# Kernel tuning notes

Hardware: AMD Instinct MI355X
Metric: run time of the kernel (lower is better)

Reference implementation:

```python
import jax, jax.numpy as jnp
import numpy as np

N_TOKENS = 2048
D_IN = 1024
D_HID = 4096
D_OUT = 1024
N_EXPERTS = 8
TOP_K = 2


def setup_inputs() -> dict:
    key = jax.random.key(0)
    ks = jax.random.split(key, 8)
    s_in = 1.0 / np.sqrt(D_IN)
    s_hid = 1.0 / np.sqrt(D_HID)
    return {
        "x": jax.random.normal(ks[0], (N_TOKENS, D_IN), dtype=jnp.float32),
        # Router Linear(D_IN, E)
        "Wr": jax.random.uniform(ks[1], (D_IN, N_EXPERTS), jnp.float32, -s_in, s_in),
        "br": jax.random.uniform(ks[2], (N_EXPERTS,), jnp.float32, -s_in, s_in),
        # Stacked expert MLP weights [E, ...]
        "W1": jax.random.uniform(ks[3], (N_EXPERTS, D_IN, D_HID), jnp.float32, -s_in, s_in),
        "b1": jax.random.uniform(ks[4], (N_EXPERTS, D_HID), jnp.float32, -s_in, s_in),
        "W2": jax.random.uniform(ks[5], (N_EXPERTS, D_HID, D_OUT), jnp.float32, -s_hid, s_hid),
        "b2": jax.random.uniform(ks[6], (N_EXPERTS, D_OUT), jnp.float32, -s_hid, s_hid),
    }


def reference(x, Wr, br, W1, b1, W2, b2):
    # Router: softmax over expert logits, then top-k
    routing = jax.nn.softmax(x @ Wr + br, axis=-1)            # [N, E]
    topk_w, topk_idx = jax.lax.top_k(routing, TOP_K)          # [N, k] each
    # Combine weights per expert: c[n, e] = sum_i topk_w[n, i] * (topk_idx[n, i] == e)
    onehot = jax.nn.one_hot(topk_idx, N_EXPERTS, dtype=x.dtype)  # [N, k, E]
    combine = jnp.einsum('nk,nke->ne', topk_w, onehot)           # [N, E]
    # Run all experts on all tokens (dense equivalent of the dispatch loop);
    # non-selected experts get combine weight 0, so math matches exactly.
    h = jax.nn.relu(jnp.einsum('nd,edh->neh', x, W1) + b1)       # [N, E, H]
    y = jnp.einsum('neh,ehd->ned', h, W2) + b2                   # [N, E, Dout]
    out = jnp.einsum('ne,ned->nd', combine, y)                   # [N, Dout]
    return out
```

## Files before the change

### kernel.cpp

```cpp
#include <hip/hip_runtime.h>
#include <hip/hip_bf16.h>

#define N_TOKENS 2048
#define D_IN 1024
#define D_HID 4096
#define D_OUT 1024
#define NE 8

typedef __attribute__((ext_vector_type(8))) short s16x8;
typedef __attribute__((ext_vector_type(4))) float f32x4;

__device__ inline unsigned short f2bf(float f) {
  union { float f; unsigned u; } v; v.f = f;
  unsigned u = v.u;
  unsigned r = u + 0x7fff + ((u >> 16) & 1);
  return (unsigned short)(r >> 16);
}

#define GLDS16(gp, lp)                                                          \
  __builtin_amdgcn_global_load_lds(                                             \
      (const __attribute__((address_space(1))) unsigned int*)(gp),              \
      (__attribute__((address_space(3))) unsigned int*)(lp), 16, 0, 0)

__global__ __launch_bounds__(256) void router_kernel(
    const float* __restrict__ x, const float* __restrict__ Wr,
    const float* __restrict__ br, int* __restrict__ cnt, int* __restrict__ tids,
    int4* __restrict__ meta, float2* __restrict__ tw) {
  int wid = threadIdx.x >> 6, lane = threadIdx.x & 63;
  int n = blockIdx.x * 4 + wid;
  const float* xr = x + (size_t)n * D_IN;
  float acc[NE];
#pragma unroll
  for (int e = 0; e < NE; e++) acc[e] = 0.f;
  for (int i = lane; i < D_IN; i += 64) {
    float xv = xr[i];
    const float4* wr = (const float4*)(Wr + (size_t)i * NE);
    float4 w0 = wr[0], w1 = wr[1];
    acc[0] += xv * w0.x; acc[1] += xv * w0.y;
    acc[2] += xv * w0.z; acc[3] += xv * w0.w;
    acc[4] += xv * w1.x; acc[5] += xv * w1.y;
    acc[6] += xv * w1.z; acc[7] += xv * w1.w;
  }
#pragma unroll
  for (int e = 0; e < NE; e++) {
#pragma unroll
    for (int s = 32; s; s >>= 1) acc[e] += __shfl_xor(acc[e], s, 64);
  }
  if (lane == 0) {
    float lg[NE], p[NE];
    float m = -1e30f;
#pragma unroll
    for (int e = 0; e < NE; e++) { lg[e] = acc[e] + br[e]; m = fmaxf(m, lg[e]); }
    float s = 0.f;
#pragma unroll
    for (int e = 0; e < NE; e++) { p[e] = expf(lg[e] - m); s += p[e]; }
    float inv = 1.f / s;
    int i0 = 0;
#pragma unroll
    for (int e = 1; e < NE; e++) if (lg[e] > lg[i0]) i0 = e;
    int i1 = (i0 == 0) ? 1 : 0;
#pragma unroll
    for (int e = 0; e < NE; e++) if (e != i0 && lg[e] > lg[i1]) i1 = e;
    int p0 = atomicAdd(&cnt[i0], 1);
    int p1 = atomicAdd(&cnt[i1], 1);
    tids[i0 * N_TOKENS + p0] = n;
    tids[i1 * N_TOKENS + p1] = n;
    meta[n] = make_int4(i0, p0, i1, p1);
    tw[n] = make_float2(p[i0] * inv, p[i1] * inv);
  }
}

__global__ __launch_bounds__(256) void convx_kernel(const float* __restrict__ x,
                                                    short* __restrict__ xb) {
  int i = (blockIdx.x * 256 + threadIdx.x) * 4;
  float4 v = *(const float4*)(x + i);
  short4 o;
  o.x = (short)f2bf(v.x); o.y = (short)f2bf(v.y);
  o.z = (short)f2bf(v.z); o.w = (short)f2bf(v.w);
  *(short4*)(xb + i) = o;
}

__global__ __launch_bounds__(256) void transconv_kernel(
    const float* __restrict__ src, short* __restrict__ dst, int R, int C) {
  __shared__ float tile[64][65];
  size_t eoff = (size_t)blockIdx.z * R * C;
  int r0 = blockIdx.y * 64, c0 = blockIdx.x * 64;
  const float* s = src + eoff + (size_t)r0 * C + c0;
  int t = threadIdx.x;
  int lc4 = (t & 15) * 4;
  int lr16 = t >> 4;
#pragma unroll
  for (int p = 0; p < 4; p++) {
    int r = p * 16 + lr16;
    float4 v = *(const float4*)(s + (size_t)r * C + lc4);
    tile[r][lc4 + 0] = v.x; tile[r][lc4 + 1] = v.y;
    tile[r][lc4 + 2] = v.z; tile[r][lc4 + 3] = v.w;
  }
  __syncthreads();
  short* d = dst + eoff + (size_t)c0 * R + r0;
  int rr4 = (t & 15) * 4;
  int cc = t >> 4;
#pragma unroll
  for (int p = 0; p < 4; p++) {
    int c = p * 16 + cc;
    short4 o;
    o.x = (short)f2bf(tile[rr4 + 0][c]);
    o.y = (short)f2bf(tile[rr4 + 1][c]);
    o.z = (short)f2bf(tile[rr4 + 2][c]);
    o.w = (short)f2bf(tile[rr4 + 3][c]);
    *(short4*)(d + (size_t)c * R + rr4) = o;
  }
}

__global__ __launch_bounds__(256) void gemm1_kernel(
    const short* __restrict__ xb,
    const short* __restrict__ W1b,
    const float* __restrict__ b1,
    const int* __restrict__ cnt, const int* __restrict__ tids,
    short* __restrict__ H) {
  const int NT_M = N_TOKENS / 128, NT_N = D_HID / 128;
  int bid0 = blockIdx.x;
  int bid = (bid0 & 7) * ((NE * NT_M * NT_N) >> 3) + (bid0 >> 3);
  int e = bid / (NT_M * NT_N);
  int r2 = bid % (NT_M * NT_N);
  int mt = r2 % NT_M, nt = r2 / NT_M;
  int ce = cnt[e];
  if (mt * 128 >= ce) return;
  int off = 0;
  for (int i = 0; i < e; i++) off += cnt[i];

  __shared__ alignas(16) short As[2][128][64];
  __shared__ alignas(16) short Bs[2][128][64];

  int lane = threadIdx.x & 63, wid = threadIdx.x >> 6;
  int wr = wid >> 1, wc = wid & 1;
  int lrow = lane >> 3;
  int ach = ((lane & 7) ^ lrow) * 8;

  const int* tlist = tids + e * N_TOKENS + mt * 128;
  const short* agp[4];
  const short* bgp[4];
#pragma unroll
  for (int c = 0; c < 4; c++) {
    int r = c * 32 + wid * 8 + lrow;
    int t = (mt * 128 + r < ce) ? tlist[r] : tlist[0];
    agp[c] = xb + (size_t)t * D_IN + ach;
    bgp[c] = W1b + (size_t)e * D_HID * D_IN + (size_t)(nt * 128 + r) * D_IN + ach;
  }

  f32x4 zero = {0.f, 0.f, 0.f, 0.f};
  f32x4 acc[4][4];
#pragma unroll
  for (int i = 0; i < 4; i++) {
#pragma unroll
    for (int j = 0; j < 4; j++) acc[i][j] = zero;
  }

#define STAGE1(ks, buf)                                                         \
  {                                                                             \
    int k0 = (ks) * 64;                                                         \
    _Pragma("unroll")                                                           \
    for (int c = 0; c < 4; c++) {                                               \
      GLDS16(agp[c] + k0, &As[buf][c * 32 + wid * 8][0]);                       \
      GLDS16(bgp[c] + k0, &Bs[buf][c * 32 + wid * 8][0]);                       \
    }                                                                           \
  }

  const int NK = D_IN / 64;
  STAGE1(0, 0);
  STAGE1(1, 1);
  int cur = 0;
  for (int ks = 0; ks < NK; ks++) {
    if (ks + 1 < NK) asm volatile("s_waitcnt vmcnt(8)" : : : "memory");
    else             asm volatile("s_waitcnt vmcnt(0)" : : : "memory");
    __builtin_amdgcn_s_barrier();
#pragma unroll
    for (int kk = 0; kk < 2; kk++) {
      s16x8 a[4], b[4];
      int ch = ((kk * 4 + (lane >> 4)) ^ (lane & 7)) * 8;
#pragma unroll
      for (int i = 0; i < 4; i++)
        a[i] = *(const s16x8*)&As[cur][wr * 64 + i * 16 + (lane & 15)][ch];
#pragma unroll
      for (int j = 0; j < 4; j++)
        b[j] = *(const s16x8*)&Bs[cur][wc * 64 + j * 16 + (lane & 15)][ch];
#pragma unroll
      for (int i = 0; i < 4; i++) {
#pragma unroll
        for (int j = 0; j < 4; j++)
          acc[i][j] = __builtin_amdgcn_mfma_f32_16x16x32_bf16(a[i], b[j], acc[i][j], 0, 0, 0);
      }
    }
    __builtin_amdgcn_s_barrier();
    if (ks + 2 < NK) STAGE1(ks + 2, cur);
    cur ^= 1;
  }

  int lr = (lane >> 4) * 4, lc = lane & 15;
#pragma unroll
  for (int j = 0; j < 4; j++) {
    int col = nt * 128 + wc * 64 + j * 16 + lc;
    float bias = b1[e * D_HID + col];
#pragma unroll
    for (int i = 0; i < 4; i++) {
#pragma unroll
      for (int r = 0; r < 4; r++) {
        int grow = mt * 128 + wr * 64 + i * 16 + lr + r;
        if (grow < ce) {
          float v = fmaxf(acc[i][j][r] + bias, 0.f);
          H[(size_t)(off + grow) * D_HID + col] = (short)f2bf(v);
        }
      }
    }
  }
}

__global__ __launch_bounds__(256) void gemm2_kernel(
    const short* __restrict__ H,
    const short* __restrict__ W2b,
    const int* __restrict__ cnt,
    float* __restrict__ Y) {
  const int NT_M = N_TOKENS / 128, NT_N = D_OUT / 128;
  int bid0 = blockIdx.x;
  int bid = (bid0 & 7) * ((NE * NT_M * NT_N) >> 3) + (bid0 >> 3);
  int e = bid / (NT_M * NT_N);
  int r2 = bid % (NT_M * NT_N);
  int mt = r2 % NT_M, nt = r2 / NT_M;
  int ce = cnt[e];
  if (mt * 128 >= ce) return;
  int off = 0;
  for (int i = 0; i < e; i++) off += cnt[i];

  __shared__ alignas(16) short As[2][128][64];
  __shared__ alignas(16) short Bs[2][128][64];

  int lane = threadIdx.x & 63, wid = threadIdx.x >> 6;
  int wr = wid >> 1, wc = wid & 1;
  int lrow = lane >> 3;
  int ach = ((lane & 7) ^ lrow) * 8;

  const short* agp[4];
  const short* bgp[4];
#pragma unroll
  for (int c = 0; c < 4; c++) {
    int r = c * 32 + wid * 8 + lrow;
    int grow = mt * 128 + r;
    if (grow > ce - 1) grow = ce - 1;
    agp[c] = H + (size_t)(off + grow) * D_HID + ach;
    bgp[c] = W2b + (size_t)e * D_OUT * D_HID + (size_t)(nt * 128 + r) * D_HID + ach;
  }

  f32x4 zero = {0.f, 0.f, 0.f, 0.f};
  f32x4 acc[4][4];
#pragma unroll
  for (int i = 0; i < 4; i++) {
#pragma unroll
    for (int j = 0; j < 4; j++) acc[i][j] = zero;
  }

#define STAGE2(ks, buf)                                                         \
  {                                                                             \
    int k0 = (ks) * 64;                                                         \
    _Pragma("unroll")                                                           \
    for (int c = 0; c < 4; c++) {                                               \
      GLDS16(agp[c] + k0, &As[buf][c * 32 + wid * 8][0]);                       \
      GLDS16(bgp[c] + k0, &Bs[buf][c * 32 + wid * 8][0]);                       \
    }                                                                           \
  }

  const int NK = D_HID / 64;
  STAGE2(0, 0);
  STAGE2(1, 1);
  int cur = 0;
  for (int ks = 0; ks < NK; ks++) {
    if (ks + 1 < NK) asm volatile("s_waitcnt vmcnt(8)" : : : "memory");
    else             asm volatile("s_waitcnt vmcnt(0)" : : : "memory");
    __builtin_amdgcn_s_barrier();
#pragma unroll
    for (int kk = 0; kk < 2; kk++) {
      s16x8 a[4], b[4];
      int ch = ((kk * 4 + (lane >> 4)) ^ (lane & 7)) * 8;
#pragma unroll
      for (int i = 0; i < 4; i++)
        a[i] = *(const s16x8*)&As[cur][wr * 64 + i * 16 + (lane & 15)][ch];
#pragma unroll
      for (int j = 0; j < 4; j++)
        b[j] = *(const s16x8*)&Bs[cur][wc * 64 + j * 16 + (lane & 15)][ch];
#pragma unroll
      for (int i = 0; i < 4; i++) {
#pragma unroll
        for (int j = 0; j < 4; j++)
          acc[i][j] = __builtin_amdgcn_mfma_f32_16x16x32_bf16(a[i], b[j], acc[i][j], 0, 0, 0);
      }
    }
    __builtin_amdgcn_s_barrier();
    if (ks + 2 < NK) STAGE2(ks + 2, cur);
    cur ^= 1;
  }

  int lr = (lane >> 4) * 4, lc = lane & 15;
#pragma unroll
  for (int j = 0; j < 4; j++) {
    int col = nt * 128 + wc * 64 + j * 16 + lc;
#pragma unroll
    for (int i = 0; i < 4; i++) {
#pragma unroll
      for (int r = 0; r < 4; r++) {
        int grow = mt * 128 + wr * 64 + i * 16 + lr + r;
        if (grow < ce) Y[(size_t)(off + grow) * D_OUT + col] = acc[i][j][r];
      }
    }
  }
}

__global__ __launch_bounds__(256) void combine_kernel(
    const float* __restrict__ Y, const float* __restrict__ b2,
    const int* __restrict__ cnt, const int4* __restrict__ meta,
    const float2* __restrict__ tw, float* __restrict__ out) {
  int n = blockIdx.x;
  int4 m = meta[n];
  float2 w = tw[n];
  int off0 = 0, off1 = 0;
#pragma unroll
  for (int i = 0; i < NE; i++) {
    int c = cnt[i];
    if (i < m.x) off0 += c;
    if (i < m.z) off1 += c;
  }
  const float4* y0 = (const float4*)(Y + (size_t)(off0 + m.y) * D_OUT);
  const float4* y1 = (const float4*)(Y + (size_t)(off1 + m.w) * D_OUT);
  const float4* g0 = (const float4*)(b2 + (size_t)m.x * D_OUT);
  const float4* g1 = (const float4*)(b2 + (size_t)m.z * D_OUT);
  float4* o = (float4*)(out + (size_t)n * D_OUT);
  int d = threadIdx.x;
  float4 a = y0[d], b = y1[d], ba = g0[d], bb = g1[d];
  float4 r;
  r.x = w.x * (a.x + ba.x) + w.y * (b.x + bb.x);
  r.y = w.x * (a.y + ba.y) + w.y * (b.y + bb.y);
  r.z = w.x * (a.z + ba.z) + w.y * (b.z + bb.z);
  r.w = w.x * (a.w + ba.w) + w.y * (b.w + bb.w);
  o[d] = r;
}

extern "C" void kernel_launch(void* const* d_in, const int* in_sizes, int n_in,
                              void* d_out, int out_size, void* d_ws, size_t ws_size,
                              hipStream_t stream) {
  const float* x  = (const float*)d_in[0];
  const float* Wr = (const float*)d_in[1];
  const float* br = (const float*)d_in[2];
  const float* W1 = (const float*)d_in[3];
  const float* b1 = (const float*)d_in[4];
  const float* W2 = (const float*)d_in[5];
  const float* b2 = (const float*)d_in[6];
  float* out = (float*)d_out;

  char* ws = (char*)d_ws;
  size_t o = 0;
  auto alloc = [&](size_t bytes) -> void* {
    o = (o + 255) & ~(size_t)255;
    void* p = ws + o;
    o += bytes;
    return p;
  };
  int*    cnt  = (int*)alloc(NE * 4);
  int*    tids = (int*)alloc((size_t)NE * N_TOKENS * 4);
  int4*   meta = (int4*)alloc((size_t)N_TOKENS * 16);
  float2* tw   = (float2*)alloc((size_t)N_TOKENS * 8);
  short*  xb   = (short*)alloc((size_t)N_TOKENS * D_IN * 2);
  short*  W1b  = (short*)alloc((size_t)NE * D_HID * D_IN * 2);
  short*  W2b  = (short*)alloc((size_t)NE * D_OUT * D_HID * 2);
  short*  H    = (short*)alloc((size_t)2 * N_TOKENS * D_HID * 2);
  float*  Y    = (float*)alloc((size_t)2 * N_TOKENS * D_OUT * 4);
  if (o > ws_size) return;

  hipMemsetAsync(cnt, 0, NE * 4, stream);
  router_kernel<<<N_TOKENS / 4, 256, 0, stream>>>(x, Wr, br, cnt, tids, meta, tw);
  convx_kernel<<<(N_TOKENS * D_IN / 4) / 256, 256, 0, stream>>>(x, xb);
  transconv_kernel<<<dim3(D_HID / 64, D_IN / 64, NE), 256, 0, stream>>>(W1, W1b, D_IN, D_HID);
  transconv_kernel<<<dim3(D_OUT / 64, D_HID / 64, NE), 256, 0, stream>>>(W2, W2b, D_HID, D_OUT);
  gemm1_kernel<<<NE * (N_TOKENS / 128) * (D_HID / 128), 256, 0, stream>>>(xb, W1b, b1, cnt, tids, H);
  gemm2_kernel<<<NE * (N_TOKENS / 128) * (D_OUT / 128), 256, 0, stream>>>(H, W2b, cnt, Y);
  combine_kernel<<<N_TOKENS, 256, 0, stream>>>(Y, b2, cnt, meta, tw, out);
}
```

Before: 579.2 us.

## Split-K gemm2 into two halves and shrink K-tile to 32

The gemm2 kernel now splits the 4096-long hidden reduction into two halves, launching twice as many blocks. Each half writes its own partial Y buffer, and the combine kernel sums the two partials. Both GEMMs also drop the LDS K-tile from 64 to 32, halving shared memory per block with a new XOR swizzle. The aim is more parallelism for the under-occupied gemm2 grid and higher occupancy. The cost is extra Y traffic, a doubled workspace, and twice as many barriers per unit of K.

```diff
diff --git a/kernel.cpp b/kernel.cpp
--- a/kernel.cpp
+++ b/kernel.cpp
@@ -129,68 +129,63 @@
   int off = 0;
   for (int i = 0; i < e; i++) off += cnt[i];
 
-  __shared__ alignas(16) short As[2][128][64];
-  __shared__ alignas(16) short Bs[2][128][64];
+  __shared__ alignas(16) short As[2][128][32];
+  __shared__ alignas(16) short Bs[2][128][32];
 
   int lane = threadIdx.x & 63, wid = threadIdx.x >> 6;
   int wr = wid >> 1, wc = wid & 1;
-  int lrow = lane >> 3;
-  int ach = ((lane & 7) ^ lrow) * 8;
+  int srow = lane >> 2;
+  int gch = ((lane & 3) ^ ((lane >> 3) & 3)) * 8;
 
   const int* tlist = tids + e * N_TOKENS + mt * 128;
-  const short* agp[4];
-  const short* bgp[4];
-#pragma unroll
-  for (int c = 0; c < 4; c++) {
-    int r = c * 32 + wid * 8 + lrow;
+  const short* a_src[2];
+  const short* b_src[2];
+#pragma unroll
+  for (int j = 0; j < 2; j++) {
+    int r = (wid + 4 * j) * 16 + srow;
     int t = (mt * 128 + r < ce) ? tlist[r] : tlist[0];
-    agp[c] = xb + (size_t)t * D_IN + ach;
-    bgp[c] = W1b + (size_t)e * D_HID * D_IN + (size_t)(nt * 128 + r) * D_IN + ach;
+    a_src[j] = xb + (size_t)t * D_IN + gch;
+    b_src[j] = W1b + (size_t)e * D_HID * D_IN + (size_t)(nt * 128 + r) * D_IN + gch;
   }
 
   f32x4 zero = {0.f, 0.f, 0.f, 0.f};
   f32x4 acc[4][4];
 #pragma unroll
-  for (int i = 0; i < 4; i++) {
+  for (int i = 0; i < 4; i++)
 #pragma unroll
     for (int j = 0; j < 4; j++) acc[i][j] = zero;
-  }
 
 #define STAGE1(ks, buf)                                                         \
   {                                                                             \
-    int k0 = (ks) * 64;                                                         \
-    _Pragma("unroll")                                                           \
-    for (int c = 0; c < 4; c++) {                                               \
-      GLDS16(agp[c] + k0, &As[buf][c * 32 + wid * 8][0]);                       \
-      GLDS16(bgp[c] + k0, &Bs[buf][c * 32 + wid * 8][0]);                       \
-    }                                                                           \
-  }
-
-  const int NK = D_IN / 64;
+    int k0 = (ks) * 32;                                                         \
+    GLDS16(a_src[0] + k0, &As[buf][wid * 16][0]);                               \
+    GLDS16(a_src[1] + k0, &As[buf][(wid + 4) * 16][0]);                         \
+    GLDS16(b_src[0] + k0, &Bs[buf][wid * 16][0]);                               \
+    GLDS16(b_src[1] + k0, &Bs[buf][(wid + 4) * 16][0]);                         \
+  }
+
+  const int NK = D_IN / 32;
   STAGE1(0, 0);
   STAGE1(1, 1);
   int cur = 0;
+  int chsh = (((lane >> 4) ^ ((lane >> 1) & 3)) & 3) * 8;
+  int arow = wr * 64 + (lane & 15), brow = wc * 64 + (lane & 15);
   for (int ks = 0; ks < NK; ks++) {
-    if (ks + 1 < NK) asm volatile("s_waitcnt vmcnt(8)" : : : "memory");
+    if (ks + 1 < NK) asm volatile("s_waitcnt vmcnt(4)" : : : "memory");
     else             asm volatile("s_waitcnt vmcnt(0)" : : : "memory");
     __builtin_amdgcn_s_barrier();
-#pragma unroll
-    for (int kk = 0; kk < 2; kk++) {
-      s16x8 a[4], b[4];
-      int ch = ((kk * 4 + (lane >> 4)) ^ (lane & 7)) * 8;
-#pragma unroll
-      for (int i = 0; i < 4; i++)
-        a[i] = *(const s16x8*)&As[cur][wr * 64 + i * 16 + (lane & 15)][ch];
+    s16x8 a[4], b[4];
+#pragma unroll
+    for (int i = 0; i < 4; i++)
+      a[i] = *(const s16x8*)&As[cur][arow + i * 16][chsh];
+#pragma unroll
+    for (int j = 0; j < 4; j++)
+      b[j] = *(const s16x8*)&Bs[cur][brow + j * 16][chsh];
+#pragma unroll
+    for (int i = 0; i < 4; i++)
 #pragma unroll
       for (int j = 0; j < 4; j++)
-        b[j] = *(const s16x8*)&Bs[cur][wc * 64 + j * 16 + (lane & 15)][ch];
-#pragma unroll
-      for (int i = 0; i < 4; i++) {
-#pragma unroll
-        for (int j = 0; j < 4; j++)
-          acc[i][j] = __builtin_amdgcn_mfma_f32_16x16x32_bf16(a[i], b[j], acc[i][j], 0, 0, 0);
-      }
-    }
+        acc[i][j] = __builtin_amdgcn_mfma_f32_16x16x32_bf16(a[i], b[j], acc[i][j], 0, 0, 0);
     __builtin_amdgcn_s_barrier();
     if (ks + 2 < NK) STAGE1(ks + 2, cur);
     cur ^= 1;
@@ -221,83 +216,83 @@
     const int* __restrict__ cnt,
     float* __restrict__ Y) {
   const int NT_M = N_TOKENS / 128, NT_N = D_OUT / 128;
+  const int PER_E = 2 * NT_M * NT_N;
   int bid0 = blockIdx.x;
-  int bid = (bid0 & 7) * ((NE * NT_M * NT_N) >> 3) + (bid0 >> 3);
-  int e = bid / (NT_M * NT_N);
-  int r2 = bid % (NT_M * NT_N);
-  int mt = r2 % NT_M, nt = r2 / NT_M;
+  int bid = (bid0 & 7) * ((NE * PER_E) >> 3) + (bid0 >> 3);
+  int e = bid / PER_E;
+  int r2 = bid % PER_E;
+  int kh = r2 / (NT_M * NT_N);
+  int r3 = r2 % (NT_M * NT_N);
+  int mt = r3 % NT_M, nt = r3 / NT_M;
   int ce = cnt[e];
   if (mt * 128 >= ce) return;
   int off = 0;
   for (int i = 0; i < e; i++) off += cnt[i];
 
-  __shared__ alignas(16) short As[2][128][64];
-  __shared__ alignas(16) short Bs[2][128][64];
+  __shared__ alignas(16) short As[2][128][32];
+  __shared__ alignas(16) short Bs[2][128][32];
 
   int lane = threadIdx.x & 63, wid = threadIdx.x >> 6;
   int wr = wid >> 1, wc = wid & 1;
-  int lrow = lane >> 3;
-  int ach = ((lane & 7) ^ lrow) * 8;
-
-  const short* agp[4];
-  const short* bgp[4];
-#pragma unroll
-  for (int c = 0; c < 4; c++) {
-    int r = c * 32 + wid * 8 + lrow;
+  int srow = lane >> 2;
+  int gch = ((lane & 3) ^ ((lane >> 3) & 3)) * 8;
+  size_t kbase = (size_t)kh * 2048;
+
+  const short* a_src[2];
+  const short* b_src[2];
+#pragma unroll
+  for (int j = 0; j < 2; j++) {
+    int r = (wid + 4 * j) * 16 + srow;
     int grow = mt * 128 + r;
     if (grow > ce - 1) grow = ce - 1;
-    agp[c] = H + (size_t)(off + grow) * D_HID + ach;
-    bgp[c] = W2b + (size_t)e * D_OUT * D_HID + (size_t)(nt * 128 + r) * D_HID + ach;
+    a_src[j] = H + (size_t)(off + grow) * D_HID + kbase + gch;
+    b_src[j] = W2b + (size_t)e * D_OUT * D_HID + (size_t)(nt * 128 + r) * D_HID + kbase + gch;
   }
 
   f32x4 zero = {0.f, 0.f, 0.f, 0.f};
   f32x4 acc[4][4];
 #pragma unroll
-  for (int i = 0; i < 4; i++) {
+  for (int i = 0; i < 4; i++)
 #pragma unroll
     for (int j = 0; j < 4; j++) acc[i][j] = zero;
-  }
 
 #define STAGE2(ks, buf)                                                         \
   {                                                                             \
-    int k0 = (ks) * 64;                                                         \
-    _Pragma("unroll")                                                           \
-    for (int c = 0; c < 4; c++) {                                               \
-      GLDS16(agp[c] + k0, &As[buf][c * 32 + wid * 8][0]);                       \
-      GLDS16(bgp[c] + k0, &Bs[buf][c * 32 + wid * 8][0]);                       \
-    }                                                                           \
-  }
-
-  const int NK = D_HID / 64;
+    int k0 = (ks) * 32;                                                         \
+    GLDS16(a_src[0] + k0, &As[buf][wid * 16][0]);                               \
+    GLDS16(a_src[1] + k0, &As[buf][(wid + 4) * 16][0]);                         \
+    GLDS16(b_src[0] + k0, &Bs[buf][wid * 16][0]);                               \
+    GLDS16(b_src[1] + k0, &Bs[buf][(wid + 4) * 16][0]);                         \
+  }
+
+  const int NK = 2048 / 32;
   STAGE2(0, 0);
   STAGE2(1, 1);
   int cur = 0;
+  int chsh = (((lane >> 4) ^ ((lane >> 1) & 3)) & 3) * 8;
+  int arow = wr * 64 + (lane & 15), brow = wc * 64 + (lane & 15);
   for (int ks = 0; ks < NK; ks++) {
-    if (ks + 1 < NK) asm volatile("s_waitcnt vmcnt(8)" : : : "memory");
+    if (ks + 1 < NK) asm volatile("s_waitcnt vmcnt(4)" : : : "memory");
     else             asm volatile("s_waitcnt vmcnt(0)" : : : "memory");
     __builtin_amdgcn_s_barrier();
-#pragma unroll
-    for (int kk = 0; kk < 2; kk++) {
-      s16x8 a[4], b[4];
-      int ch = ((kk * 4 + (lane >> 4)) ^ (lane & 7)) * 8;
-#pragma unroll
-      for (int i = 0; i < 4; i++)
-        a[i] = *(const s16x8*)&As[cur][wr * 64 + i * 16 + (lane & 15)][ch];
+    s16x8 a[4], b[4];
+#pragma unroll
+    for (int i = 0; i < 4; i++)
+      a[i] = *(const s16x8*)&As[cur][arow + i * 16][chsh];
+#pragma unroll
+    for (int j = 0; j < 4; j++)
+      b[j] = *(const s16x8*)&Bs[cur][brow + j * 16][chsh];
+#pragma unroll
+    for (int i = 0; i < 4; i++)
 #pragma unroll
       for (int j = 0; j < 4; j++)
-        b[j] = *(const s16x8*)&Bs[cur][wc * 64 + j * 16 + (lane & 15)][ch];
-#pragma unroll
-      for (int i = 0; i < 4; i++) {
-#pragma unroll
-        for (int j = 0; j < 4; j++)
-          acc[i][j] = __builtin_amdgcn_mfma_f32_16x16x32_bf16(a[i], b[j], acc[i][j], 0, 0, 0);
-      }
-    }
+        acc[i][j] = __builtin_amdgcn_mfma_f32_16x16x32_bf16(a[i], b[j], acc[i][j], 0, 0, 0);
     __builtin_amdgcn_s_barrier();
     if (ks + 2 < NK) STAGE2(ks + 2, cur);
     cur ^= 1;
   }
 
+  float* Yh = Y + (size_t)kh * (2 * N_TOKENS) * D_OUT;
   int lr = (lane >> 4) * 4, lc = lane & 15;
 #pragma unroll
   for (int j = 0; j < 4; j++) {
@@ -307,7 +302,7 @@
 #pragma unroll
       for (int r = 0; r < 4; r++) {
         int grow = mt * 128 + wr * 64 + i * 16 + lr + r;
-        if (grow < ce) Y[(size_t)(off + grow) * D_OUT + col] = acc[i][j][r];
+        if (grow < ce) Yh[(size_t)(off + grow) * D_OUT + col] = acc[i][j][r];
       }
     }
   }
@@ -317,6 +312,7 @@
     const float* __restrict__ Y, const float* __restrict__ b2,
     const int* __restrict__ cnt, const int4* __restrict__ meta,
     const float2* __restrict__ tw, float* __restrict__ out) {
+  const size_t YH = (size_t)(2 * N_TOKENS) * D_OUT;
   int n = blockIdx.x;
   int4 m = meta[n];
   float2 w = tw[n];
@@ -327,18 +323,23 @@
     if (i < m.x) off0 += c;
     if (i < m.z) off1 += c;
   }
-  const float4* y0 = (const float4*)(Y + (size_t)(off0 + m.y) * D_OUT);
-  const float4* y1 = (const float4*)(Y + (size_t)(off1 + m.w) * D_OUT);
+  size_t r0 = (size_t)(off0 + m.y) * D_OUT;
+  size_t r1 = (size_t)(off1 + m.w) * D_OUT;
+  const float4* y0a = (const float4*)(Y + r0);
+  const float4* y0b = (const float4*)(Y + YH + r0);
+  const float4* y1a = (const float4*)(Y + r1);
+  const float4* y1b = (const float4*)(Y + YH + r1);
   const float4* g0 = (const float4*)(b2 + (size_t)m.x * D_OUT);
   const float4* g1 = (const float4*)(b2 + (size_t)m.z * D_OUT);
   float4* o = (float4*)(out + (size_t)n * D_OUT);
   int d = threadIdx.x;
-  float4 a = y0[d], b = y1[d], ba = g0[d], bb = g1[d];
+  float4 a0 = y0a[d], a1 = y0b[d], b0 = y1a[d], b1v = y1b[d];
+  float4 ba = g0[d], bb = g1[d];
   float4 r;
-  r.x = w.x * (a.x + ba.x) + w.y * (b.x + bb.x);
-  r.y = w.x * (a.y + ba.y) + w.y * (b.y + bb.y);
-  r.z = w.x * (a.z + ba.z) + w.y * (b.z + bb.z);
-  r.w = w.x * (a.w + ba.w) + w.y * (b.w + bb.w);
+  r.x = w.x * (a0.x + a1.x + ba.x) + w.y * (b0.x + b1v.x + bb.x);
+  r.y = w.x * (a0.y + a1.y + ba.y) + w.y * (b0.y + b1v.y + bb.y);
+  r.z = w.x * (a0.z + a1.z + ba.z) + w.y * (b0.z + b1v.z + bb.z);
+  r.w = w.x * (a0.w + a1.w + ba.w) + w.y * (b0.w + b1v.w + bb.w);
   o[d] = r;
 }
 
@@ -370,7 +371,7 @@
   short*  W1b  = (short*)alloc((size_t)NE * D_HID * D_IN * 2);
   short*  W2b  = (short*)alloc((size_t)NE * D_OUT * D_HID * 2);
   short*  H    = (short*)alloc((size_t)2 * N_TOKENS * D_HID * 2);
-  float*  Y    = (float*)alloc((size_t)2 * N_TOKENS * D_OUT * 4);
+  float*  Y    = (float*)alloc((size_t)2 * 2 * N_TOKENS * D_OUT * 4);
   if (o > ws_size) return;
 
   hipMemsetAsync(cnt, 0, NE * 4, stream);
@@ -379,6 +380,6 @@
   transconv_kernel<<<dim3(D_HID / 64, D_IN / 64, NE), 256, 0, stream>>>(W1, W1b, D_IN, D_HID);
   transconv_kernel<<<dim3(D_OUT / 64, D_HID / 64, NE), 256, 0, stream>>>(W2, W2b, D_HID, D_OUT);
   gemm1_kernel<<<NE * (N_TOKENS / 128) * (D_HID / 128), 256, 0, stream>>>(xb, W1b, b1, cnt, tids, H);
-  gemm2_kernel<<<NE * (N_TOKENS / 128) * (D_OUT / 128), 256, 0, stream>>>(H, W2b, cnt, Y);
+  gemm2_kernel<<<NE * (N_TOKENS / 128) * (D_OUT / 128) * 2, 256, 0, stream>>>(H, W2b, cnt, Y);
   combine_kernel<<<N_TOKENS, 256, 0, stream>>>(Y, b2, cnt, meta, tw, out);
 }
```

After: 564.2 us. -2.6%, faster.
